# Optimization experiments

Measured on AMD Instinct MI355X. Metric: run time of the kernel, lower is better.

## Reference

```python
import jax, jax.numpy as jnp
import numpy as np

# dims: F=N_fault, V=N_train (noise samples), E=batch, M=n_in+2, N=n_out
F, V, E, N_IN, N_OUT = 2, 4, 2048, 512, 512
M = N_IN + 2
GMIN, GMAX, EPS_TRAIN, PGMIN = 0.01, 10.0, 0.1, 1e-4
ETA2_ACT1 = 0.20  # ACT1.eta_fault[0,2], used in theta init
# pTanh activation params per ACT: a = e0 + e1*tanh((z-e2)*e3)
ETAS = np.array([[0.05, 0.90, 0.20, 8.0],
                 [0.10, 0.80, 0.30, 5.0],
                 [0.00, 1.00, 0.25, 10.0],
                 [0.15, 0.70, 0.15, 6.0]], dtype=np.float32)


def setup_inputs() -> dict:
    key = jax.random.key(0)
    k1, k2, k3, k4, k5 = jax.random.split(key, 5)
    a_previous = jax.random.uniform(k1, (F, V, E, N_IN), jnp.float32)
    # theta init per __init__: rand/100 + gmin; last row += gmax; row -2 from eta_2 formula
    theta = jax.random.uniform(k2, (M, N_OUT), jnp.float32) / 100.0 + GMIN
    theta = theta.at[-1, :].add(GMAX)
    theta = theta.at[-2, :].set(ETA2_ACT1 / (1.0 - ETA2_ACT1) * (jnp.sum(theta[:-2, :], 0) + theta[-1, :]))
    cofficients_act = jax.random.uniform(k3, (4, N_OUT), jnp.float32)
    noise_u = jax.random.uniform(k4, (F, V, M, N_OUT), jnp.float32)   # theta_noisy uniform draw
    gumbel_u = jax.random.uniform(k5, (4, N_OUT), jnp.float32)        # gumbel uniform draw
    return {"a_previous": a_previous, "theta_": theta,
            "cofficients_act": cofficients_act, "noise_u": noise_u, "gumbel_u": gumbel_u}


def _forward(a_previous, theta_, cofficients_act, noise_u, gumbel_u):
    sg = jax.lax.stop_gradient
    # --- theta property: clamp to [-gmax,gmax], zero |.|<gmin, straight-through ---
    th_c = jnp.clip(theta_, -GMAX, GMAX)
    th_t = jnp.where(jnp.abs(th_c) < GMIN, 0.0, th_c)
    theta = sg(th_t) + theta_ - sg(theta_)
    # --- theta_noisy: multiplicative uniform noise in [1-eps, 1+eps]; FaultMask == 1 ---
    theta_noisy = theta[None, None] * ((noise_u * 2.0 - 1.0) * EPS_TRAIN + 1.0)  # [F,V,M,N]
    absn = jnp.abs(theta_noisy)
    W = absn / (jnp.sum(absn, axis=2, keepdims=True) + 1e-10)
    pos = (theta_noisy >= 0).astype(theta_noisy.dtype)
    neg = 1.0 - pos
    # --- MAC: extend input with [ones, zeros], inverter path, split-sign matmul ---
    ones = jnp.ones(a_previous.shape[:3] + (1,), a_previous.dtype)
    zeros = jnp.zeros_like(ones)
    x_ext = jnp.concatenate([a_previous, ones, zeros], axis=3)  # [F,V,E,M]
    x_neg = (-x_ext).at[..., -1].set(0.0)                       # ideal INV(a) = -a, last col zeroed
    z = (jnp.einsum('fvem,fvmn->fven', x_ext, W * pos)
         + jnp.einsum('fvem,fvmn->fven', x_neg, W * neg))       # [F,V,E,N]
    # --- MAC_power: vectorized form of the quad loop ---
    # Power = sum_{f,v,m,n} g[m,n] * sum_e (x_ext*pos + x_neg*neg - y)^2 / (E*V*F)
    # pos*neg = 0, pos^2 = pos  =>  expand the square into einsum reductions.
    g_init = jnp.abs(th_c)
    g_tilde = g_init * (PGMIN / jnp.min(g_init, axis=0, keepdims=True))
    pos_d, neg_d = sg(pos), sg(neg)  # detached in torch source
    sx2 = jnp.einsum('fvem,fvem->fvm', x_ext, x_ext)
    sn2 = jnp.einsum('fvem,fvem->fvm', x_neg, x_neg)
    sy2 = jnp.einsum('fven,fven->fvn', z, z)
    C = jnp.einsum('fvem,fven->fvmn', x_ext, z)
    D = jnp.einsum('fvem,fven->fvmn', x_neg, z)
    p1 = (jnp.einsum('fvm,fvmn,mn->', sx2, pos_d, g_tilde)
          + jnp.einsum('fvm,fvmn,mn->', sn2, neg_d, g_tilde))
    p2 = -2.0 * (jnp.einsum('fvmn,fvmn,mn->', C, pos_d, g_tilde)
                 + jnp.einsum('fvmn,fvmn,mn->', D, neg_d, g_tilde))
    p3 = jnp.einsum('fvn,n->', sy2, jnp.sum(g_tilde, axis=0))
    mac_power = (p1 + p2 + p3) / (E * V * F)
    # --- CoFF_ACT: clamped logits + gumbel, softmax, hard argmax straight-through ---
    c = cofficients_act + sg(jnp.clip(cofficients_act, -1.0, 1.0) - cofficients_act)
    gn = -jnp.log(-jnp.log(gumbel_u + 1e-20) + 1e-20)
    alpha = jax.nn.softmax((c + gn) / 1.0, axis=0)              # temperature = 1.0
    hard = jax.nn.one_hot(jnp.argmax(alpha, axis=0), 4, axis=0, dtype=alpha.dtype)
    alpha_st = sg(hard) + alpha - sg(alpha)                      # [4, N]
    # --- mix the four pTanh activations ---
    a_new = jnp.zeros_like(z)
    for i in range(4):
        e0, e1, e2, e3 = ETAS[i]
        a_new = a_new + alpha_st[i] * (e0 + e1 * jnp.tanh((z - e2) * e3))
    return a_new, mac_power


def reference(a_previous, theta_, cofficients_act, noise_u, gumbel_u):
    return _forward(a_previous, theta_, cofficients_act, noise_u, gumbel_u)
```

## Files before the change

### kernel.cpp

```cpp
#include <hip/hip_runtime.h>

typedef unsigned short u16;
typedef __attribute__((ext_vector_type(8))) short short8;
typedef __attribute__((ext_vector_type(4))) float f32x4;

#define NF 2
#define NV 4
#define FV 8
#define NE 2048
#define NIN 512
#define NOUT 512
#define NM 514

#define WS_P1      0u
#define WS_P2      2048u
#define WS_P3      3072u
#define WS_SCALE   4224u
#define WS_G       6272u
#define WS_GN      8448u
#define WS_ETA     10496u
#define WS_BIASZ   18688u
#define WS_BIAST   35072u
#define WS_DENP    51456u
#define WS_PMIN    182528u
#define WS_PSUM    313600u
#define WS_ABF     444672u
#define WS_BZT     17221888u
#define WS_BTT     21416192u

__constant__ float c_etas[4][4] = {
    {0.05f, 0.90f, 0.20f, 8.0f},
    {0.10f, 0.80f, 0.30f, 5.0f},
    {0.00f, 1.00f, 0.25f, 10.0f},
    {0.15f, 0.70f, 0.15f, 6.0f}};

__device__ __forceinline__ u16 f2bf(float x) {
    unsigned u = __float_as_uint(x);
    unsigned r = (u + 0x7fffu + ((u >> 16) & 1u)) >> 16;
    return (u16)r;
}

__device__ __forceinline__ void gll16(const void* g, void* l) {
    __builtin_amdgcn_global_load_lds((__attribute__((address_space(1))) void*)g,
                                     (__attribute__((address_space(3))) void*)l,
                                     16, 0, 0);
}

__global__ void kA_part(const float* __restrict__ theta_, float* __restrict__ pmin,
                        float* __restrict__ psum, float* __restrict__ wszero) {
    int t = threadIdx.x;
    if (blockIdx.x == 0) {
        for (int i = t; i < 2112; i += 256) wszero[i] = 0.f;
    }
    int n2 = t * 2;
    int r0 = blockIdx.x * 33;
    float mn0 = 3.4e38f, mn1 = 3.4e38f, s0 = 0.f, s1 = 0.f;
    int rend = r0 + 33;
    if (rend > NM) rend = NM;
    for (int r = r0; r < rend; r++) {
        float2 v = *(const float2*)(theta_ + r * NOUT + n2);
        float a0 = fabsf(fminf(fmaxf(v.x, -10.f), 10.f));
        float a1 = fabsf(fminf(fmaxf(v.y, -10.f), 10.f));
        mn0 = fminf(mn0, a0); mn1 = fminf(mn1, a1);
        s0 += a0; s1 += a1;
    }
    *(float2*)(pmin + blockIdx.x * NOUT + n2) = make_float2(mn0, mn1);
    *(float2*)(psum + blockIdx.x * NOUT + n2) = make_float2(s0, s1);
}

__global__ void k_wmat3(const float* __restrict__ theta_,
                        const float* __restrict__ pmin, const float* __restrict__ psum,
                        const float* __restrict__ coeff, const float* __restrict__ gumb,
                        const float* __restrict__ noise,
                        u16* __restrict__ BzT, u16* __restrict__ BtT,
                        float* __restrict__ bias_z, float* __restrict__ bias_t,
                        float* __restrict__ denomp, float* __restrict__ G,
                        float* __restrict__ Gn, float4* __restrict__ eta4) {
    const int nt = blockIdx.x, mt = blockIdx.y, fv = blockIdx.z;
    const int t = threadIdx.x;
    const int nq = t & 15, mr = t >> 4;
    const int nb = nt * 64 + nq * 4;
    __shared__ u16 Wl[64][72];
    __shared__ u16 Sl[64][72];
    __shared__ float4 red[16][17];
    float4 mn4 = {3.4e38f, 3.4e38f, 3.4e38f, 3.4e38f};
#pragma unroll
    for (int i = 0; i < 16; i++) {
        float4 v = *(const float4*)(pmin + i * NOUT + nb);
        mn4.x = fminf(mn4.x, v.x); mn4.y = fminf(mn4.y, v.y);
        mn4.z = fminf(mn4.z, v.z); mn4.w = fminf(mn4.w, v.w);
    }
    float4 sc4 = {1e-4f / mn4.x, 1e-4f / mn4.y, 1e-4f / mn4.z, 1e-4f / mn4.w};
    float4 dacc = {0.f, 0.f, 0.f, 0.f};
#pragma unroll
    for (int i = 0; i < 4; i++) {
        int ml = mr + i * 16;
        int m = mt * 64 + ml;
        float4 th4 = *(const float4*)(theta_ + m * NOUT + nb);
        float4 no4 = *(const float4*)(noise + (fv * NM + m) * NOUT + nb);
        ushort4 wv, sv;
        float gs = 0.f;
#define WCOMP(c, fld) { float fac = no4.c * 0.2f + 0.9f; \
                        float thc = fminf(fmaxf(th4.c, -10.f), 10.f); \
                        float gi = fabsf(thc); \
                        float tht = (gi < 0.01f) ? 0.f : thc; \
                        float th = tht * fac; \
                        wv.fld = f2bf(th); \
                        sv.fld = f2bf(((th >= 0.f) ? gi : -gi) * sc4.c); \
                        gs += gi * sc4.c; \
                        dacc.c += fabsf(th); }
        WCOMP(x, x) WCOMP(y, y) WCOMP(z, z) WCOMP(w, w)
#undef WCOMP
        *(ushort4*)(&Wl[ml][nq * 4]) = wv;
        *(ushort4*)(&Sl[ml][nq * 4]) = sv;
        if (fv == 0) {
            gs += __shfl_xor(gs, 1);
            gs += __shfl_xor(gs, 2);
            gs += __shfl_xor(gs, 4);
            gs += __shfl_xor(gs, 8);
            if (nq == 0) atomicAdd(&G[m], gs);
        }
    }
    red[mr][nq] = dacc;
    __syncthreads();
    if (t < 16) {
        float4 s = red[0][t];
#pragma unroll
        for (int r = 1; r < 16; r++) {
            float4 v = red[r][t];
            s.x += v.x; s.y += v.y; s.z += v.z; s.w += v.w;
        }
        *(float4*)(denomp + (mt * 8 + fv) * NOUT + nt * 64 + t * 4) = s;
    }
    const int mb = (t & 15) * 4;
#pragma unroll
    for (int r = 0; r < 4; r++) {
        int nl = (t >> 4) + r * 16;
        ushort4 wv, sv;
        wv.x = Wl[mb][nl]; wv.y = Wl[mb + 1][nl]; wv.z = Wl[mb + 2][nl]; wv.w = Wl[mb + 3][nl];
        sv.x = Sl[mb][nl]; sv.y = Sl[mb + 1][nl]; sv.z = Sl[mb + 2][nl]; sv.w = Sl[mb + 3][nl];
        int gidx = (fv * NOUT + nt * 64 + nl) * NIN + mt * 64 + mb;
        *(ushort4*)(BzT + gidx) = wv;
        *(ushort4*)(BtT + gidx) = sv;
    }
    if (mt == 0 && t < 64) {
        int n = nt * 64 + t;
        float mn = 3.4e38f, s = 0.f;
#pragma unroll
        for (int i = 0; i < 16; i++) {
            mn = fminf(mn, pmin[i * NOUT + n]);
            s += psum[i * NOUT + n];
        }
        float sc = 1e-4f / mn;
        float fac = noise[(fv * NM + 512) * NOUT + n] * 0.2f + 0.9f;
        float thc = fminf(fmaxf(theta_[512 * NOUT + n], -10.f), 10.f);
        float gi = fabsf(thc);
        float tht = (gi < 0.01f) ? 0.f : thc;
        float th = tht * fac;
        bias_z[fv * NOUT + n] = th;
        bias_t[fv * NOUT + n] = ((th >= 0.f) ? gi : -gi) * sc;
        if (fv == 0) {
            float gsb = gi * sc;
            for (int off = 32; off > 0; off >>= 1) gsb += __shfl_down(gsb, off);
            if (t == 0) atomicAdd(&G[512], gsb);
        }
        Gn[n] = sc * s;
        float best = -1e30f;
        int bi = 0;
#pragma unroll
        for (int i = 0; i < 4; i++) {
            float c = fminf(fmaxf(coeff[i * NOUT + n], -1.f), 1.f);
            float u = gumb[i * NOUT + n];
            float g = -logf(-logf(u + 1e-20f) + 1e-20f);
            float v = c + g;
            if (v > best) { best = v; bi = i; }
        }
        eta4[n] = make_float4(c_etas[bi][0], c_etas[bi][1], c_etas[bi][2], c_etas[bi][3]);
    }
}

__global__ void k_prepA(const float* __restrict__ a_prev, const float* __restrict__ G,
                        u16* __restrict__ Abf, float* __restrict__ p1slot) {
    int t = threadIdx.x;
    float acc = 0.f;
#pragma unroll
    for (int i = 0; i < 4; i++) {
        int idx = (i * 2048 + blockIdx.x) * 256 + t;
        float4 v = ((const float4*)a_prev)[idx];
        int k = (idx & 127) << 2;
        float4 g4 = *((const float4*)(G + k));
        acc += v.x * v.x * g4.x + v.y * v.y * g4.y + v.z * v.z * g4.z + v.w * v.w * g4.w;
        ushort4 o;
        o.x = f2bf(v.x); o.y = f2bf(v.y); o.z = f2bf(v.z); o.w = f2bf(v.w);
        ((ushort4*)Abf)[idx] = o;
    }
    for (int off = 32; off > 0; off >>= 1) acc += __shfl_down(acc, off);
    __shared__ float red[4];
    int lane = t & 63, wv = t >> 6;
    if (lane == 0) red[wv] = acc;
    __syncthreads();
    if (t == 0)
        atomicAdd(&p1slot[(blockIdx.x & 63) * 8], red[0] + red[1] + red[2] + red[3]);
}

__global__ __launch_bounds__(256, 2) void k_gemm(
    const u16* __restrict__ Abf, const u16* __restrict__ BzT, const u16* __restrict__ BtT,
    const float* __restrict__ bias_z, const float* __restrict__ bias_t,
    const float* __restrict__ Gn, const float4* __restrict__ eta4,
    const float* __restrict__ theta_, const float* __restrict__ noise,
    const float* __restrict__ denomp,
    float* __restrict__ out, float* __restrict__ p2slot, float* __restrict__ p3slot) {
    __shared__ alignas(16) u16 As[128 * 64];
    __shared__ alignas(16) u16 Bzs[128 * 64];
    __shared__ alignas(16) u16 Bts[128 * 64];
    const int tid = threadIdx.x;
    const int lane = tid & 63;
    const int wv = tid >> 6;
    const int wr = wv >> 1, wc = wv & 1;
    const int b = blockIdx.x;
    const int fv = b & 7;
    const int kk = b >> 3;
    const int n0 = (kk & 3) * 128;
    const int e0 = (kk >> 2) * 128;

    const u16* Ag = Abf + (fv * NE + e0) * NIN;
    const u16* Bzg = BzT + (fv * NOUT + n0) * NIN;
    const u16* Btg = BtT + (fv * NOUT + n0) * NIN;

    f32x4 accz[4][4], acct[4][4];
#pragma unroll
    for (int i = 0; i < 4; i++)
#pragma unroll
        for (int j = 0; j < 4; j++) {
            f32x4 zz = {0.f, 0.f, 0.f, 0.f};
            accz[i][j] = zz;
            acct[i][j] = zz;
        }

    const int srow = tid >> 3;
    const int swz = (((tid & 7) ^ (srow & 7))) * 8;

    for (int k0 = 0; k0 < 512; k0 += 64) {
#pragma unroll
        for (int i = 0; i < 4; i++) {
            int so = (i * 32 + srow) * 512 + k0 + swz;
            int dof = i * 2048 + tid * 8;
            gll16(Ag + so, (u16*)As + dof);
            gll16(Bzg + so, (u16*)Bzs + dof);
            gll16(Btg + so, (u16*)Bts + dof);
        }
        __builtin_amdgcn_s_waitcnt(0);
        __syncthreads();
        const int rA = wr * 64 + (lane & 15);
        const int rB = wc * 64 + (lane & 15);
#pragma unroll
        for (int s = 0; s < 2; s++) {
            const int ca = ((s * 4 + (lane >> 4)) ^ (lane & 7)) * 8;
            short8 af[4], bzf[4], btf[4];
#pragma unroll
            for (int i = 0; i < 4; i++) af[i] = *(const short8*)(As + (rA + i * 16) * 64 + ca);
#pragma unroll
            for (int j = 0; j < 4; j++) {
                bzf[j] = *(const short8*)(Bzs + (rB + j * 16) * 64 + ca);
                btf[j] = *(const short8*)(Bts + (rB + j * 16) * 64 + ca);
            }
#pragma unroll
            for (int i = 0; i < 4; i++)
#pragma unroll
                for (int j = 0; j < 4; j++) {
                    accz[i][j] = __builtin_amdgcn_mfma_f32_16x16x32_bf16(af[i], bzf[j], accz[i][j], 0, 0, 0);
                    acct[i][j] = __builtin_amdgcn_mfma_f32_16x16x32_bf16(af[i], btf[j], acct[i][j], 0, 0, 0);
                }
        }
        __syncthreads();
    }

    float p2 = 0.f, p3 = 0.f;
    const int col = lane & 15;
    const int rowq = (lane >> 4) * 4;
#pragma unroll
    for (int j = 0; j < 4; j++) {
        int n = n0 + wc * 64 + j * 16 + col;
        float dsum = 1e-10f;
#pragma unroll
        for (int mc = 0; mc < 8; mc++) dsum += denomp[(mc * 8 + fv) * NOUT + n];
#pragma unroll
        for (int mx = 512; mx < 514; mx++) {
            float fac = noise[(fv * NM + mx) * NOUT + n] * 0.2f + 0.9f;
            float thc = fminf(fmaxf(theta_[mx * NOUT + n], -10.f), 10.f);
            float tht = (fabsf(thc) < 0.01f) ? 0.f : thc;
            dsum += fabsf(tht * fac);
        }
        float rdv = 1.f / dsum;
        float bz = bias_z[fv * NOUT + n];
        float bt = bias_t[fv * NOUT + n];
        float gnv = Gn[n];
        float4 e4 = eta4[n];
#pragma unroll
        for (int i = 0; i < 4; i++) {
            int ebase = e0 + wr * 64 + i * 16 + rowq;
#pragma unroll
            for (int r = 0; r < 4; r++) {
                float z = (accz[i][j][r] + bz) * rdv;
                float t = acct[i][j][r] + bt;
                p2 += z * t;
                p3 += z * z * gnv;
                float x = (z - e4.z) * e4.w;
                float ex = __expf(2.f * x);
                float th = 1.f - 2.f / (ex + 1.f);
                out[(fv * NE + ebase + r) * NOUT + n] = e4.x + e4.y * th;
            }
        }
    }
    for (int off = 32; off > 0; off >>= 1) {
        p2 += __shfl_down(p2, off);
        p3 += __shfl_down(p3, off);
    }
    __shared__ float r2[4], r3[4];
    if (lane == 0) { r2[wv] = p2; r3[wv] = p3; }
    __syncthreads();
    if (tid == 0) {
        int slot = (b & 31) * 8;
        atomicAdd(&p2slot[slot], r2[0] + r2[1] + r2[2] + r2[3]);
        atomicAdd(&p3slot[slot], r3[0] + r3[1] + r3[2] + r3[3]);
    }
}

__global__ void k_final(const float* __restrict__ p1s, const float* __restrict__ p2s,
                        const float* __restrict__ p3s, const float* __restrict__ G,
                        float* __restrict__ out) {
    int t = threadIdx.x;
    float s1 = p1s[t * 8];
    float s2 = (t < 32) ? p2s[t * 8] : 0.f;
    float s3 = (t < 32) ? p3s[t * 8] : 0.f;
    for (int off = 32; off > 0; off >>= 1) {
        s1 += __shfl_down(s1, off);
        s2 += __shfl_down(s2, off);
        s3 += __shfl_down(s3, off);
    }
    if (t == 0) {
        float mp = (s1 + 16384.f * G[512] - 2.f * s2 + s3) * (1.f / 16384.f);
        out[8388608] = mp;
    }
}

extern "C" void kernel_launch(void* const* d_in, const int* in_sizes, int n_in,
                              void* d_out, int out_size, void* d_ws, size_t ws_size,
                              hipStream_t stream) {
    const float* a_prev = (const float*)d_in[0];
    const float* theta_ = (const float*)d_in[1];
    const float* coeff = (const float*)d_in[2];
    const float* noise = (const float*)d_in[3];
    const float* gumb = (const float*)d_in[4];
    float* out = (float*)d_out;
    char* w = (char*)d_ws;
    float* p1s = (float*)(w + WS_P1);
    float* p2s = (float*)(w + WS_P2);
    float* p3s = (float*)(w + WS_P3);
    float* G = (float*)(w + WS_G);
    float* Gn = (float*)(w + WS_GN);
    float4* eta4 = (float4*)(w + WS_ETA);
    float* bias_z = (float*)(w + WS_BIASZ);
    float* bias_t = (float*)(w + WS_BIAST);
    float* denomp = (float*)(w + WS_DENP);
    float* pmin = (float*)(w + WS_PMIN);
    float* psum = (float*)(w + WS_PSUM);
    u16* Abf = (u16*)(w + WS_ABF);
    u16* BzT = (u16*)(w + WS_BZT);
    u16* BtT = (u16*)(w + WS_BTT);

    kA_part<<<16, 256, 0, stream>>>(theta_, pmin, psum, (float*)w);
    k_wmat3<<<dim3(8, 8, FV), 256, 0, stream>>>(theta_, pmin, psum, coeff, gumb, noise,
                                                BzT, BtT, bias_z, bias_t, denomp, G,
                                                Gn, eta4);
    k_prepA<<<2048, 256, 0, stream>>>(a_prev, G, Abf, p1s);
    k_gemm<<<512, 256, 0, stream>>>(Abf, BzT, BtT, bias_z, bias_t, Gn, eta4,
                                    theta_, noise, denomp, out, p2s, p3s);
    k_final<<<1, 64, 0, stream>>>(p1s, p2s, p3s, G, out);
}
```

Baseline: 138.9 us.

## Double-buffer GEMM LDS tiles with K=32 stages to overlap loads and MFMA

The GEMM main loop moves from a single 64-wide K tile, loaded then waited on in full, to two 32-wide LDS buffers. The next stage's global-to-LDS loads are issued while MFMAs run on the current stage, and a partial vmcnt wait replaces the full drain. The aim is to hide global memory latency behind compute. It costs an extra barrier per step, a new swizzle pattern for the narrower tiles, and more sensitivity to getting the manual waitcnt and barrier ordering right.

```diff
diff --git a/kernel.cpp b/kernel.cpp
--- a/kernel.cpp
+++ b/kernel.cpp
@@ -210,9 +210,9 @@
     const float* __restrict__ theta_, const float* __restrict__ noise,
     const float* __restrict__ denomp,
     float* __restrict__ out, float* __restrict__ p2slot, float* __restrict__ p3slot) {
-    __shared__ alignas(16) u16 As[128 * 64];
-    __shared__ alignas(16) u16 Bzs[128 * 64];
-    __shared__ alignas(16) u16 Bts[128 * 64];
+    __shared__ alignas(16) u16 As[2 * 128 * 32];
+    __shared__ alignas(16) u16 Bzs[2 * 128 * 32];
+    __shared__ alignas(16) u16 Bts[2 * 128 * 32];
     const int tid = threadIdx.x;
     const int lane = tid & 63;
     const int wv = tid >> 6;
@@ -237,43 +237,82 @@
             acct[i][j] = zz;
         }
 
-    const int srow = tid >> 3;
-    const int swz = (((tid & 7) ^ (srow & 7))) * 8;
-
-    for (int k0 = 0; k0 < 512; k0 += 64) {
+    int soff[2];
+#pragma unroll
+    for (int h = 0; h < 2; h++) {
+        int row = h * 64 + (tid >> 2);
+        int g = (tid & 3) ^ ((row ^ (row >> 2)) & 3);
+        soff[h] = row * 512 + g * 8;
+    }
+    const int dof = tid * 8;
+
+#define STAGE(buf, k0)                                                        \
+    {                                                                         \
+        _Pragma("unroll") for (int h = 0; h < 2; h++) {                       \
+            int d = (buf) * 4096 + h * 2048 + dof;                            \
+            gll16(Ag + soff[h] + (k0), (u16*)As + d);                         \
+            gll16(Bzg + soff[h] + (k0), (u16*)Bzs + d);                       \
+            gll16(Btg + soff[h] + (k0), (u16*)Bts + d);                       \
+        }                                                                     \
+    }
+
+    const int l4 = lane & 15;
+    const int swr = (l4 ^ (l4 >> 2)) & 3;
+    const int sl = ((lane >> 4) ^ swr) * 8;
+    const int rdA = (wr * 64 + l4) * 32 + sl;
+    const int rdB = (wc * 64 + l4) * 32 + sl;
+
+    STAGE(0, 0)
+    STAGE(1, 32)
+
+    int k0 = 0;
+    for (int step = 0; step < 15; step++, k0 += 32) {
+        const int buf = step & 1;
+        asm volatile("s_waitcnt vmcnt(6)" ::: "memory");
+        __builtin_amdgcn_s_barrier();
+        asm volatile("" ::: "memory");
+        short8 af[4], bzf[4], btf[4];
+        const int bo = buf * 4096;
 #pragma unroll
         for (int i = 0; i < 4; i++) {
-            int so = (i * 32 + srow) * 512 + k0 + swz;
-            int dof = i * 2048 + tid * 8;
-            gll16(Ag + so, (u16*)As + dof);
-            gll16(Bzg + so, (u16*)Bzs + dof);
-            gll16(Btg + so, (u16*)Bts + dof);
-        }
-        __builtin_amdgcn_s_waitcnt(0);
-        __syncthreads();
-        const int rA = wr * 64 + (lane & 15);
-        const int rB = wc * 64 + (lane & 15);
-#pragma unroll
-        for (int s = 0; s < 2; s++) {
-            const int ca = ((s * 4 + (lane >> 4)) ^ (lane & 7)) * 8;
-            short8 af[4], bzf[4], btf[4];
-#pragma unroll
-            for (int i = 0; i < 4; i++) af[i] = *(const short8*)(As + (rA + i * 16) * 64 + ca);
+            af[i] = *(const short8*)(As + bo + rdA + i * 512);
+            bzf[i] = *(const short8*)(Bzs + bo + rdB + i * 512);
+            btf[i] = *(const short8*)(Bts + bo + rdB + i * 512);
+        }
+        asm volatile("s_waitcnt lgkmcnt(0)" ::: "memory");
+        __builtin_amdgcn_sched_barrier(0);
+        __builtin_amdgcn_s_barrier();
+        asm volatile("" ::: "memory");
+        if (step < 14) STAGE(buf, k0 + 64)
+#pragma unroll
+        for (int i = 0; i < 4; i++)
 #pragma unroll
             for (int j = 0; j < 4; j++) {
-                bzf[j] = *(const short8*)(Bzs + (rB + j * 16) * 64 + ca);
-                btf[j] = *(const short8*)(Bts + (rB + j * 16) * 64 + ca);
+                accz[i][j] = __builtin_amdgcn_mfma_f32_16x16x32_bf16(af[i], bzf[j], accz[i][j], 0, 0, 0);
+                acct[i][j] = __builtin_amdgcn_mfma_f32_16x16x32_bf16(af[i], btf[j], acct[i][j], 0, 0, 0);
             }
-#pragma unroll
-            for (int i = 0; i < 4; i++)
-#pragma unroll
-                for (int j = 0; j < 4; j++) {
-                    accz[i][j] = __builtin_amdgcn_mfma_f32_16x16x32_bf16(af[i], bzf[j], accz[i][j], 0, 0, 0);
-                    acct[i][j] = __builtin_amdgcn_mfma_f32_16x16x32_bf16(af[i], btf[j], acct[i][j], 0, 0, 0);
-                }
-        }
-        __syncthreads();
-    }
+    }
+    {
+        asm volatile("s_waitcnt vmcnt(0)" ::: "memory");
+        __builtin_amdgcn_s_barrier();
+        asm volatile("" ::: "memory");
+        short8 af[4], bzf[4], btf[4];
+        const int bo = 4096;
+#pragma unroll
+        for (int i = 0; i < 4; i++) {
+            af[i] = *(const short8*)(As + bo + rdA + i * 512);
+            bzf[i] = *(const short8*)(Bzs + bo + rdB + i * 512);
+            btf[i] = *(const short8*)(Bts + bo + rdB + i * 512);
+        }
+#pragma unroll
+        for (int i = 0; i < 4; i++)
+#pragma unroll
+            for (int j = 0; j < 4; j++) {
+                accz[i][j] = __builtin_amdgcn_mfma_f32_16x16x32_bf16(af[i], bzf[j], accz[i][j], 0, 0, 0);
+                acct[i][j] = __builtin_amdgcn_mfma_f32_16x16x32_bf16(af[i], btf[j], acct[i][j], 0, 0, 0);
+            }
+    }
+#undef STAGE
 
     float p2 = 0.f, p3 = 0.f;
     const int col = lane & 15;
```

Result: no change. 141.5 us (+1.9%).

## Merge A-conversion into weight-prep kernel and defer G-weighting of p1

Applied to the files above, without the earlier changes.

The bf16 conversion of a_previous is merged into the weight-matrix preparation kernel as extra blocks of one launch, removing a separate kernel and its dependency on G. Instead of weighting squared inputs by G during conversion, per-column sums of squares are accumulated into eight slot copies with atomics, and the G-weighted reduction moves into the final kernel. This lets the memory-bound conversion overlap with weight preparation and removes one launch, at the cost of many more atomics and a larger final-reduction kernel.

```diff
diff --git a/kernel.cpp b/kernel.cpp
--- a/kernel.cpp
+++ b/kernel.cpp
@@ -27,6 +27,7 @@
 #define WS_ABF     444672u
 #define WS_BZT     17221888u
 #define WS_BTT     21416192u
+#define WS_S8      25610496u
 
 __constant__ float c_etas[4][4] = {
     {0.05f, 0.90f, 0.20f, 8.0f},
@@ -47,10 +48,14 @@
 }
 
 __global__ void kA_part(const float* __restrict__ theta_, float* __restrict__ pmin,
-                        float* __restrict__ psum, float* __restrict__ wszero) {
+                        float* __restrict__ psum, float* __restrict__ wszero,
+                        float* __restrict__ S8) {
     int t = threadIdx.x;
     if (blockIdx.x == 0) {
         for (int i = t; i < 2112; i += 256) wszero[i] = 0.f;
+    }
+    if (blockIdx.x == 1) {
+        for (int i = t; i < 4096; i += 256) S8[i] = 0.f;
     }
     int n2 = t * 2;
     int r0 = blockIdx.x * 33;
@@ -68,21 +73,54 @@
     *(float2*)(psum + blockIdx.x * NOUT + n2) = make_float2(s0, s1);
 }
 
-__global__ void k_wmat3(const float* __restrict__ theta_,
-                        const float* __restrict__ pmin, const float* __restrict__ psum,
-                        const float* __restrict__ coeff, const float* __restrict__ gumb,
-                        const float* __restrict__ noise,
-                        u16* __restrict__ BzT, u16* __restrict__ BtT,
-                        float* __restrict__ bias_z, float* __restrict__ bias_t,
-                        float* __restrict__ denomp, float* __restrict__ G,
-                        float* __restrict__ Gn, float4* __restrict__ eta4) {
-    const int nt = blockIdx.x, mt = blockIdx.y, fv = blockIdx.z;
-    const int t = threadIdx.x;
-    const int nq = t & 15, mr = t >> 4;
-    const int nb = nt * 64 + nq * 4;
+__global__ void k_mid(const float* __restrict__ theta_,
+                      const float* __restrict__ pmin, const float* __restrict__ psum,
+                      const float* __restrict__ coeff, const float* __restrict__ gumb,
+                      const float* __restrict__ noise, const float* __restrict__ a_prev,
+                      u16* __restrict__ BzT, u16* __restrict__ BtT,
+                      u16* __restrict__ Abf,
+                      float* __restrict__ bias_z, float* __restrict__ bias_t,
+                      float* __restrict__ denomp, float* __restrict__ G,
+                      float* __restrict__ Gn, float4* __restrict__ eta4,
+                      float* __restrict__ S8) {
     __shared__ u16 Wl[64][72];
     __shared__ u16 Sl[64][72];
     __shared__ float4 red[16][17];
+    const int t = threadIdx.x;
+    const int bid = blockIdx.x;
+
+    if (bid < 512) {
+        const int b = bid;
+        float4 sacc = {0.f, 0.f, 0.f, 0.f};
+#pragma unroll
+        for (int i = 0; i < 16; i++) {
+            int idx = (i * 512 + b) * 256 + t;
+            float4 v = ((const float4*)a_prev)[idx];
+            sacc.x += v.x * v.x; sacc.y += v.y * v.y;
+            sacc.z += v.z * v.z; sacc.w += v.w * v.w;
+            ushort4 o;
+            o.x = f2bf(v.x); o.y = f2bf(v.y); o.z = f2bf(v.z); o.w = f2bf(v.w);
+            ((ushort4*)Abf)[idx] = o;
+        }
+        float4* sred = (float4*)Wl;
+        if (t >= 128) sred[t - 128] = sacc;
+        __syncthreads();
+        if (t < 128) {
+            float4 p = sred[t];
+            sacc.x += p.x; sacc.y += p.y; sacc.z += p.z; sacc.w += p.w;
+            float* dst = S8 + (b & 7) * 512 + t * 4;
+            atomicAdd(dst + 0, sacc.x);
+            atomicAdd(dst + 1, sacc.y);
+            atomicAdd(dst + 2, sacc.z);
+            atomicAdd(dst + 3, sacc.w);
+        }
+        return;
+    }
+
+    const int wb = bid - 512;
+    const int nt = wb & 7, mt = (wb >> 3) & 7, fv = wb >> 6;
+    const int nq = t & 15, mr = t >> 4;
+    const int nb = nt * 64 + nq * 4;
     float4 mn4 = {3.4e38f, 3.4e38f, 3.4e38f, 3.4e38f};
 #pragma unroll
     for (int i = 0; i < 16; i++) {
@@ -179,30 +217,6 @@
     }
 }
 
-__global__ void k_prepA(const float* __restrict__ a_prev, const float* __restrict__ G,
-                        u16* __restrict__ Abf, float* __restrict__ p1slot) {
-    int t = threadIdx.x;
-    float acc = 0.f;
-#pragma unroll
-    for (int i = 0; i < 4; i++) {
-        int idx = (i * 2048 + blockIdx.x) * 256 + t;
-        float4 v = ((const float4*)a_prev)[idx];
-        int k = (idx & 127) << 2;
-        float4 g4 = *((const float4*)(G + k));
-        acc += v.x * v.x * g4.x + v.y * v.y * g4.y + v.z * v.z * g4.z + v.w * v.w * g4.w;
-        ushort4 o;
-        o.x = f2bf(v.x); o.y = f2bf(v.y); o.z = f2bf(v.z); o.w = f2bf(v.w);
-        ((ushort4*)Abf)[idx] = o;
-    }
-    for (int off = 32; off > 0; off >>= 1) acc += __shfl_down(acc, off);
-    __shared__ float red[4];
-    int lane = t & 63, wv = t >> 6;
-    if (lane == 0) red[wv] = acc;
-    __syncthreads();
-    if (t == 0)
-        atomicAdd(&p1slot[(blockIdx.x & 63) * 8], red[0] + red[1] + red[2] + red[3]);
-}
-
 __global__ __launch_bounds__(256, 2) void k_gemm(
     const u16* __restrict__ Abf, const u16* __restrict__ BzT, const u16* __restrict__ BtT,
     const float* __restrict__ bias_z, const float* __restrict__ bias_t,
@@ -326,21 +340,33 @@
     }
 }
 
-__global__ void k_final(const float* __restrict__ p1s, const float* __restrict__ p2s,
+__global__ void k_final(const float* __restrict__ S8, const float* __restrict__ p2s,
                         const float* __restrict__ p3s, const float* __restrict__ G,
                         float* __restrict__ out) {
     int t = threadIdx.x;
-    float s1 = p1s[t * 8];
-    float s2 = (t < 32) ? p2s[t * 8] : 0.f;
-    float s3 = (t < 32) ? p3s[t * 8] : 0.f;
-    for (int off = 32; off > 0; off >>= 1) {
-        s1 += __shfl_down(s1, off);
-        s2 += __shfl_down(s2, off);
-        s3 += __shfl_down(s3, off);
-    }
-    if (t == 0) {
-        float mp = (s1 + 16384.f * G[512] - 2.f * s2 + s3) * (1.f / 16384.f);
-        out[8388608] = mp;
+    float ss = 0.f;
+#pragma unroll
+    for (int s = 0; s < 8; s++) ss += S8[s * 512 + t];
+    float s1 = G[t] * ss;
+    for (int off = 32; off > 0; off >>= 1) s1 += __shfl_down(s1, off);
+    __shared__ float r1[8];
+    int lane = t & 63, w = t >> 6;
+    if (lane == 0) r1[w] = s1;
+    __syncthreads();
+    if (t < 64) {
+        float s2 = (t < 32) ? p2s[t * 8] : 0.f;
+        float s3 = (t < 32) ? p3s[t * 8] : 0.f;
+        for (int off = 32; off > 0; off >>= 1) {
+            s2 += __shfl_down(s2, off);
+            s3 += __shfl_down(s3, off);
+        }
+        if (t == 0) {
+            float s1t = 0.f;
+#pragma unroll
+            for (int q = 0; q < 8; q++) s1t += r1[q];
+            float mp = (s1t + 16384.f * G[512] - 2.f * s2 + s3) * (1.f / 16384.f);
+            out[8388608] = mp;
+        }
     }
 }
 
@@ -354,7 +380,6 @@
     const float* gumb = (const float*)d_in[4];
     float* out = (float*)d_out;
     char* w = (char*)d_ws;
-    float* p1s = (float*)(w + WS_P1);
     float* p2s = (float*)(w + WS_P2);
     float* p3s = (float*)(w + WS_P3);
     float* G = (float*)(w + WS_G);
@@ -368,13 +393,12 @@
     u16* Abf = (u16*)(w + WS_ABF);
     u16* BzT = (u16*)(w + WS_BZT);
     u16* BtT = (u16*)(w + WS_BTT);
-
-    kA_part<<<16, 256, 0, stream>>>(theta_, pmin, psum, (float*)w);
-    k_wmat3<<<dim3(8, 8, FV), 256, 0, stream>>>(theta_, pmin, psum, coeff, gumb, noise,
-                                                BzT, BtT, bias_z, bias_t, denomp, G,
-                                                Gn, eta4);
-    k_prepA<<<2048, 256, 0, stream>>>(a_prev, G, Abf, p1s);
+    float* S8 = (float*)(w + WS_S8);
+
+    kA_part<<<16, 256, 0, stream>>>(theta_, pmin, psum, (float*)w, S8);
+    k_mid<<<1024, 256, 0, stream>>>(theta_, pmin, psum, coeff, gumb, noise, a_prev,
+                                    BzT, BtT, Abf, bias_z, bias_t, denomp, G, Gn, eta4, S8);
     k_gemm<<<512, 256, 0, stream>>>(Abf, BzT, BtT, bias_z, bias_t, Gn, eta4,
                                     theta_, noise, denomp, out, p2s, p3s);
-    k_final<<<1, 64, 0, stream>>>(p1s, p2s, p3s, G, out);
-}
+    k_final<<<1, 512, 0, stream>>>(S8, p2s, p3s, G, out);
+}
```

Result: no change. 140.6 us (+1.2%).
